# Kernel tuning notes

Measured on AMD Instinct MI355X. Metric: run time of the kernel, lower is better.

The kernel has to match this reference:

```python
import jax, jax.numpy as jnp
import numpy as np

B, S, E = 2, 2048, 2048
A, H = 2048, 16  # attention_dim, n_heads
HD = A // H      # head_dim = 128
ROPE_THETA = 10000.0


def setup_inputs() -> dict:
    key = jax.random.key(0)
    k1, k2, k3 = jax.random.split(key, 3)
    x = jax.random.normal(k1, (B, S, E), dtype=jnp.float32)
    W_qkv = jax.random.normal(k2, (E, 3 * A), dtype=jnp.float32) * 0.02
    W_out = jax.random.normal(k3, (A, E), dtype=jnp.float32) * 0.02
    return {"x": x, "W_qkv": W_qkv, "W_out": W_out}


def _apply_rope(x):
    # x: (B, H, S, D); interleaved rotary pairs (rotary-embedding-torch default)
    b, h, s, d = x.shape
    inv_freq = 1.0 / (ROPE_THETA ** (jnp.arange(0, d, 2, dtype=jnp.float32) / d))
    freqs = jnp.arange(s, dtype=jnp.float32)[:, None] * inv_freq[None, :]  # (S, D/2)
    cos, sin = jnp.cos(freqs), jnp.sin(freqs)
    xr = x.reshape(b, h, s, d // 2, 2)
    x1, x2 = xr[..., 0], xr[..., 1]
    o1 = x1 * cos - x2 * sin
    o2 = x1 * sin + x2 * cos
    return jnp.stack([o1, o2], axis=-1).reshape(b, h, s, d)


def reference(x, W_qkv, W_out):
    b, s, _ = x.shape
    qkv = (x @ W_qkv).reshape(b, s, 3, H, HD)          # (B,S,3,H,hd)
    qkv = jnp.moveaxis(qkv, 3, 1)                      # movedim(-2,1) -> (B,H,S,3,hd)
    q, k, v = qkv[..., 0, :], qkv[..., 1, :], qkv[..., 2, :]
    q = _apply_rope(q)
    k = _apply_rope(k)
    scale = 1.0 / jnp.sqrt(jnp.asarray(HD, dtype=x.dtype))
    scores = jnp.einsum("bhqd,bhkd->bhqk", q, k) * scale
    attn = jax.nn.softmax(scores, axis=-1)
    out = jnp.einsum("bhqk,bhkd->bhqd", attn, v)       # (B,H,S,hd)
    out = out.transpose(0, 2, 1, 3).reshape(b, s, A)   # (B,S,A)
    return out @ W_out
```

## Files before the change

### kernel.cpp

```cpp
#include <hip/hip_runtime.h>
#include <math.h>

typedef float  f32x4 __attribute__((ext_vector_type(4)));
typedef short  s16x8 __attribute__((ext_vector_type(8)));
typedef short  s16x4 __attribute__((ext_vector_type(4)));
typedef unsigned short u16;
typedef unsigned int u32;

static __device__ __forceinline__ u16 f32_to_bf16_rne(float f) {
    u32 u = __builtin_bit_cast(u32, f);
    u32 r = u + 0x7fffu + ((u >> 16) & 1u);
    return (u16)(r >> 16);
}
static __device__ __forceinline__ u32 pack_bf16_rhu(float a, float b) {
    u32 ua = __builtin_bit_cast(u32, a);
    u32 ub = __builtin_bit_cast(u32, b);
    return ((ua + 0x8000u) >> 16) | ((ub + 0x8000u) & 0xffff0000u);
}
static __device__ __forceinline__ float bf16_to_f32(u16 h) {
    return __builtin_bit_cast(float, (u32)h << 16);
}

static __device__ __forceinline__ void gl2lds16(const void* g, void* l) {
    __builtin_amdgcn_global_load_lds(
        (const __attribute__((address_space(1))) u32*)g,
        (__attribute__((address_space(3))) u32*)l, 16, 0, 0);
}

__global__ __launch_bounds__(256) void k_cast(const float* __restrict__ in,
                                              u16* __restrict__ out) {
    int i = (blockIdx.x * 256 + threadIdx.x) * 8;
    float4 a = *reinterpret_cast<const float4*>(in + i);
    float4 b = *reinterpret_cast<const float4*>(in + i + 4);
    s16x8 o;
    o[0] = (short)f32_to_bf16_rne(a.x); o[1] = (short)f32_to_bf16_rne(a.y);
    o[2] = (short)f32_to_bf16_rne(a.z); o[3] = (short)f32_to_bf16_rne(a.w);
    o[4] = (short)f32_to_bf16_rne(b.x); o[5] = (short)f32_to_bf16_rne(b.y);
    o[6] = (short)f32_to_bf16_rne(b.z); o[7] = (short)f32_to_bf16_rne(b.w);
    *reinterpret_cast<s16x8*>(out + i) = o;
}

__global__ __launch_bounds__(256) void k_transpose_cast(const float* __restrict__ in,
                                                        u16* __restrict__ out,
                                                        int R, int C) {
    __shared__ float TT[64 * 130];
    const int t = threadIdx.x;
    const int ct = blockIdx.x, rt = blockIdx.y;
    const int tr = t >> 4;
    const int tc = t & 15;
    float4 v[8];
#pragma unroll
    for (int u = 0; u < 8; ++u) {
        int r = u * 16 + tr;
        v[u] = *reinterpret_cast<const float4*>(in + (size_t)(rt * 128 + r) * C + ct * 64 + tc * 4);
    }
#pragma unroll
    for (int u = 0; u < 8; ++u) {
        int r = u * 16 + tr;
        TT[(tc * 4 + 0) * 130 + r] = v[u].x;
        TT[(tc * 4 + 1) * 130 + r] = v[u].y;
        TT[(tc * 4 + 2) * 130 + r] = v[u].z;
        TT[(tc * 4 + 3) * 130 + r] = v[u].w;
    }
    __syncthreads();
#pragma unroll
    for (int u = 0; u < 4; ++u) {
        int oc = u * 16 + tr;
        int r0 = tc * 8;
        s16x8 o;
#pragma unroll
        for (int e = 0; e < 8; ++e)
            o[e] = (short)f32_to_bf16_rne(TT[oc * 130 + r0 + e]);
        *reinterpret_cast<s16x8*>(out + (size_t)(ct * 64 + oc) * R + rt * 128 + r0) = o;
    }
}

template<bool BF16OUT, bool ROPE>
__global__ __launch_bounds__(256) void k_gemm_bt(const u16* __restrict__ Amat,
                                                 const u16* __restrict__ Bt,
                                                 void* __restrict__ Cout,
                                                 int M, int N, int K) {
    __shared__ __align__(16) u16 As[128 * 64];
    __shared__ __align__(16) u16 Bs[128 * 64];
    const int t = threadIdx.x;
    const int lane = t & 63, wave = t >> 6;
    const int m16 = lane & 15, qd = lane >> 4;
    const int wm = (wave >> 1) * 64, wn = (wave & 1) * 64;
    const size_t m0 = (size_t)blockIdx.y * 128, n0 = (size_t)blockIdx.x * 128;
    const int srow = lane >> 3;
    const int schunk = (lane & 7) ^ srow;

    f32x4 acc[4][4] = {};

    for (int k0 = 0; k0 < K; k0 += 64) {
#pragma unroll
        for (int j = 0; j < 4; ++j) {
            int rbase = j * 32 + wave * 8;
            int r = rbase + srow;
            gl2lds16(Amat + (m0 + r) * (size_t)K + k0 + schunk * 8, &As[rbase * 64]);
            gl2lds16(Bt   + (n0 + r) * (size_t)K + k0 + schunk * 8, &Bs[rbase * 64]);
        }
        __syncthreads();
#pragma unroll
        for (int kh = 0; kh < 2; ++kh) {
            s16x8 af[4], bf[4];
#pragma unroll
            for (int i = 0; i < 4; ++i) {
                int ra = wm + i * 16 + m16;
                int pa = (kh * 4 + qd) ^ (ra & 7);
                af[i] = *reinterpret_cast<const s16x8*>(&As[ra * 64 + pa * 8]);
                int rb = wn + i * 16 + m16;
                int pb = (kh * 4 + qd) ^ (rb & 7);
                bf[i] = *reinterpret_cast<const s16x8*>(&Bs[rb * 64 + pb * 8]);
            }
#pragma unroll
            for (int i = 0; i < 4; ++i)
#pragma unroll
                for (int jj = 0; jj < 4; ++jj)
                    acc[i][jj] = __builtin_amdgcn_mfma_f32_16x16x32_bf16(af[i], bf[jj], acc[i][jj], 0, 0, 0);
        }
        __syncthreads();
    }
    if (ROPE && n0 < 4096) {
        float invf[4];
#pragma unroll
        for (int j = 0; j < 4; ++j) {
            int pi = ((int)(wn + j * 16 + m16) & 127) >> 1;
            invf[j] = __expf(-0.14391156831f * (float)pi);
        }
#pragma unroll
        for (int i = 0; i < 4; ++i)
#pragma unroll
            for (int j = 0; j < 4; ++j)
#pragma unroll
                for (int r = 0; r < 4; ++r) {
                    float v = acc[i][j][r];
                    float p = __shfl_xor(v, 1);
                    size_t row = m0 + wm + i * 16 + qd * 4 + r;
                    float f = (float)(int)(row & 2047) * invf[j];
                    float sn, cs;
                    __sincosf(f, &sn, &cs);
                    float res = (m16 & 1) ? fmaf(p, sn, v * cs) : fmaf(v, cs, -p * sn);
                    size_t col = n0 + wn + j * 16 + m16;
                    ((u16*)Cout)[row * N + col] = f32_to_bf16_rne(res);
                }
    } else {
#pragma unroll
        for (int i = 0; i < 4; ++i)
#pragma unroll
            for (int j = 0; j < 4; ++j)
#pragma unroll
                for (int r = 0; r < 4; ++r) {
                    size_t row = m0 + wm + i * 16 + qd * 4 + r;
                    size_t col = n0 + wn + j * 16 + m16;
                    if (BF16OUT)
                        ((u16*)Cout)[row * N + col] = f32_to_bf16_rne(acc[i][j][r]);
                    else
                        ((float*)Cout)[row * N + col] = acc[i][j][r];
                }
    }
}

__global__ __launch_bounds__(256) void k_transpose_v(const u16* __restrict__ qkv,
                                                     u16* __restrict__ vt) {
    __shared__ u16 TT[128 * 130];
    const int t = threadIdx.x;
    const int st = blockIdx.x;
    const int bh = blockIdx.y;
    const int b = bh >> 4, h = bh & 15;
    const u16* src = qkv + (size_t)b * 2048 * 6144 + 4096 + (size_t)h * 128;
    const int tr = t >> 4, tc = t & 15;
    s16x8 v[8];
#pragma unroll
    for (int u = 0; u < 8; ++u) {
        int s = u * 16 + tr;
        v[u] = *reinterpret_cast<const s16x8*>(src + (size_t)(st * 128 + s) * 6144 + tc * 8);
    }
#pragma unroll
    for (int u = 0; u < 8; ++u) {
        int s = u * 16 + tr;
#pragma unroll
        for (int e = 0; e < 8; ++e)
            TT[(tc * 8 + e) * 130 + s] = (u16)v[u][e];
    }
    __syncthreads();
    u16* dst = vt + (size_t)bh * 128 * 2048 + st * 128;
#pragma unroll
    for (int u = 0; u < 8; ++u) {
        int d = u * 16 + tr;
        int s0 = tc * 8;
        s16x8 o;
#pragma unroll
        for (int e = 0; e < 8; ++e) o[e] = (short)TT[d * 130 + s0 + e];
        *reinterpret_cast<s16x8*>(dst + (size_t)d * 2048 + s0) = o;
    }
}

__global__ __launch_bounds__(512, 4) void k_flash(const u16* __restrict__ qkv,
                                                  const u16* __restrict__ vt,
                                                  u16* __restrict__ out) {
    __shared__ __align__(16) u16 KS[128 * 136];
    __shared__ __align__(16) u16 VS[128 * 136];
    const int t = threadIdx.x, lane = t & 63, wave = t >> 6;
    const int m16 = lane & 15, qd = lane >> 4;
    const int bh = blockIdx.y, b = bh >> 4, h = bh & 15;
    const int q0 = blockIdx.x * 128;
    const u16* Qg = qkv + (size_t)b * 2048 * 6144 + (size_t)h * 128;
    const u16* Kg = Qg + 2048;
    const u16* Vtg = vt + (size_t)bh * 128 * 2048;
    const float C2 = 0.12751743f;

    int srow[4], scol[4], pi0[4];
#pragma unroll
    for (int ci = 0; ci < 4; ++ci) {
        int idx = ci * 512 + t;
        int row = idx >> 4, c = idx & 15;
        srow[ci] = row;
        scol[ci] = c * 8;
        pi0[ci] = 32 * (c >> 2) + 16 * (c & 1) + 4 * ((c >> 1) & 1);
    }

    s16x8 qf[4];
#pragma unroll
    for (int kc = 0; kc < 4; ++kc)
        qf[kc] = *reinterpret_cast<const s16x8*>(
            Qg + (size_t)(q0 + wave * 16 + m16) * 6144 + kc * 32 + qd * 8);

    f32x4 accO[8] = {};
    float mrow = -1e30f, lrow = 0.f;

    for (int kt = 0; kt < 16; ++kt) {
        const int s0 = kt * 128;
        s16x8 kreg[4], vreg[4];
#pragma unroll
        for (int ci = 0; ci < 4; ++ci) {
            kreg[ci] = *reinterpret_cast<const s16x8*>(
                Kg + (size_t)(s0 + srow[ci]) * 6144 + scol[ci]);
            vreg[ci] = *reinterpret_cast<const s16x8*>(
                Vtg + (size_t)srow[ci] * 2048 + s0 + scol[ci]);
        }
        __syncthreads();
#pragma unroll
        for (int ci = 0; ci < 4; ++ci) {
            *reinterpret_cast<s16x8*>(&KS[srow[ci] * 136 + scol[ci]]) = kreg[ci];
            s16x4 lo = __builtin_shufflevector(vreg[ci], vreg[ci], 0, 1, 2, 3);
            s16x4 hi = __builtin_shufflevector(vreg[ci], vreg[ci], 4, 5, 6, 7);
            *reinterpret_cast<s16x4*>(&VS[srow[ci] * 136 + pi0[ci]]) = lo;
            *reinterpret_cast<s16x4*>(&VS[srow[ci] * 136 + pi0[ci] + 8]) = hi;
        }
        __syncthreads();

        f32x4 accS[8] = {};
#pragma unroll
        for (int kc = 0; kc < 4; ++kc)
#pragma unroll
            for (int nj = 0; nj < 8; ++nj) {
                s16x8 kf = *reinterpret_cast<const s16x8*>(
                    &KS[(nj * 16 + m16) * 136 + (kc * 4 + qd) * 8]);
                accS[nj] = __builtin_amdgcn_mfma_f32_16x16x32_bf16(kf, qf[kc], accS[nj], 0, 0, 0);
            }

        float mx = accS[0][0];
#pragma unroll
        for (int nj = 0; nj < 8; ++nj)
#pragma unroll
            for (int r = 0; r < 4; ++r) mx = fmaxf(mx, accS[nj][r]);
        mx *= C2;
        mx = fmaxf(mx, __shfl_xor(mx, 16));
        mx = fmaxf(mx, __shfl_xor(mx, 32));
        float mn = fmaxf(mrow, mx);
        float alpha = __builtin_amdgcn_exp2f(mrow - mn);
        mrow = mn;
        float ls = 0.f;
        s16x4 pk[8];
#pragma unroll
        for (int nj = 0; nj < 8; ++nj) {
            float p0 = __builtin_amdgcn_exp2f(fmaf(accS[nj][0], C2, -mn));
            float p1 = __builtin_amdgcn_exp2f(fmaf(accS[nj][1], C2, -mn));
            float p2 = __builtin_amdgcn_exp2f(fmaf(accS[nj][2], C2, -mn));
            float p3 = __builtin_amdgcn_exp2f(fmaf(accS[nj][3], C2, -mn));
            ls += (p0 + p1) + (p2 + p3);
            u32 lo = pack_bf16_rhu(p0, p1);
            u32 hi = pack_bf16_rhu(p2, p3);
            uint2 pr = make_uint2(lo, hi);
            pk[nj] = __builtin_bit_cast(s16x4, pr);
        }
        ls += __shfl_xor(ls, 16);
        ls += __shfl_xor(ls, 32);
        lrow = lrow * alpha + ls;
        float aO[4];
#pragma unroll
        for (int r = 0; r < 4; ++r) aO[r] = __shfl(alpha, qd * 4 + r);
#pragma unroll
        for (int dj = 0; dj < 8; ++dj)
#pragma unroll
            for (int r = 0; r < 4; ++r) accO[dj][r] *= aO[r];

#pragma unroll
        for (int kb = 0; kb < 4; ++kb) {
            s16x8 af = __builtin_shufflevector(pk[2 * kb], pk[2 * kb + 1],
                                               0, 1, 2, 3, 4, 5, 6, 7);
#pragma unroll
            for (int dj = 0; dj < 8; ++dj) {
                s16x8 vf = *reinterpret_cast<const s16x8*>(
                    &VS[(dj * 16 + m16) * 136 + kb * 32 + qd * 8]);
                accO[dj] = __builtin_amdgcn_mfma_f32_16x16x32_bf16(af, vf, accO[dj], 0, 0, 0);
            }
        }
    }
    float invl = 1.0f / lrow;
    float iv[4];
#pragma unroll
    for (int r = 0; r < 4; ++r) iv[r] = __shfl(invl, qd * 4 + r);
#pragma unroll
    for (int r = 0; r < 4; ++r) {
        size_t row = (size_t)b * 2048 + q0 + wave * 16 + qd * 4 + r;
#pragma unroll
        for (int dj = 0; dj < 8; ++dj)
            out[row * 2048 + h * 128 + dj * 16 + m16] =
                f32_to_bf16_rne(accO[dj][r] * iv[r]);
    }
}

extern "C" void kernel_launch(void* const* d_in, const int* in_sizes, int n_in,
                              void* d_out, int out_size, void* d_ws, size_t ws_size,
                              hipStream_t stream) {
    const float* x     = (const float*)d_in[0];
    const float* W_qkv = (const float*)d_in[1];
    const float* W_out = (const float*)d_in[2];
    float* out = (float*)d_out;

    char* ws = (char*)d_ws;
    u16* xb   = (u16*)(ws);
    u16* Wqt  = (u16*)(ws + (16u << 20));
    u16* Wot  = (u16*)(ws + (40u << 20));
    u16* qkvb = (u16*)(ws + (48u << 20));
    u16* attn = (u16*)(ws + (96u << 20));
    u16* vtg  = (u16*)(ws + (112u << 20));

    k_cast<<<4096, 256, 0, stream>>>(x, xb);
    k_transpose_cast<<<dim3(96, 16), 256, 0, stream>>>(W_qkv, Wqt, 2048, 6144);
    k_transpose_cast<<<dim3(32, 16), 256, 0, stream>>>(W_out, Wot, 2048, 2048);
    k_gemm_bt<true, true><<<dim3(48, 32), 256, 0, stream>>>(xb, Wqt, qkvb, 4096, 6144, 2048);
    k_transpose_v<<<dim3(16, 32), 256, 0, stream>>>(qkvb, vtg);
    k_flash<<<dim3(16, 32), 512, 0, stream>>>(qkvb, vtg, attn);
    k_gemm_bt<false, false><<<dim3(16, 32), 256, 0, stream>>>(attn, Wot, out, 4096, 2048, 2048);
}
```

Baseline: 409.3 us.

## Add 256x256-tile 8-wave GEMM with staged LDS pipeline for QKV projection

```diff
diff --git a/kernel.cpp b/kernel.cpp
--- a/kernel.cpp
+++ b/kernel.cpp
@@ -161,6 +161,187 @@
     }
 }
 
+template<bool BF16OUT, bool ROPE>
+__global__ __launch_bounds__(512) void k_gemm256(const u16* __restrict__ Amat,
+                                                 const u16* __restrict__ Bt,
+                                                 void* __restrict__ Cout,
+                                                 int M, int N, int K) {
+    __shared__ __align__(16) u16 As[2][256 * 64];
+    __shared__ __align__(16) u16 Bs[2][256 * 64];
+    const int t = threadIdx.x;
+    const int lane = t & 63, wave = t >> 6;
+    const int m16 = lane & 15, qd = lane >> 4;
+    const int wr = wave >> 2, wc = wave & 3;
+    const int srow = lane >> 3;
+    const int sch = (lane & 7) ^ srow;
+
+    const int nwg = gridDim.x * gridDim.y;
+    int orig = blockIdx.y * gridDim.x + blockIdx.x;
+    int qq = nwg >> 3, rr = nwg & 7;
+    int xcd = orig & 7, loc = orig >> 3;
+    int wg = (xcd < rr ? xcd * (qq + 1) : rr * (qq + 1) + (xcd - rr) * qq) + loc;
+    int bx = wg % gridDim.x, by = wg / gridDim.x;
+    const size_t m0 = (size_t)by * 256, n0 = (size_t)bx * 256;
+
+    const u16* Ab = Amat + m0 * (size_t)K;
+    const u16* Bb = Bt + n0 * (size_t)K;
+    const int NT = K >> 6;
+
+    auto stageA = [&](int p, int h, int k0) {
+        int rb0 = h * 128 + wave * 8;
+        gl2lds16(Ab + (size_t)(rb0 + srow) * K + k0 + sch * 8, &As[p][rb0 * 64]);
+        int rb1 = rb0 + 64;
+        gl2lds16(Ab + (size_t)(rb1 + srow) * K + k0 + sch * 8, &As[p][rb1 * 64]);
+    };
+    auto stageB = [&](int p, int h, int k0) {
+        int rb0 = h * 128 + wave * 8;
+        gl2lds16(Bb + (size_t)(rb0 + srow) * K + k0 + sch * 8, &Bs[p][rb0 * 64]);
+        int rb1 = rb0 + 64;
+        gl2lds16(Bb + (size_t)(rb1 + srow) * K + k0 + sch * 8, &Bs[p][rb1 * 64]);
+    };
+
+    f32x4 acc[8][4] = {};
+    s16x8 af[4][2], bq0[2][2], bq1[2][2];
+
+    stageA(0, 0, 0); stageA(0, 1, 0);
+    stageB(0, 0, 0); stageB(0, 1, 0);
+    if (NT > 1) {
+        stageB(1, 0, 64); stageB(1, 1, 64);
+        asm volatile("s_waitcnt vmcnt(4)" ::: "memory");
+    } else {
+        asm volatile("s_waitcnt vmcnt(0)" ::: "memory");
+    }
+    __builtin_amdgcn_s_barrier();
+
+    for (int kt = 0; kt < NT; ++kt) {
+        const int p = kt & 1;
+        const int rowA = wr * 128;
+
+#pragma unroll
+        for (int i = 0; i < 4; ++i) {
+            int ra = rowA + i * 16 + m16;
+            af[i][0] = *reinterpret_cast<const s16x8*>(&As[p][ra * 64 + ((qd)     ^ (ra & 7)) * 8]);
+            af[i][1] = *reinterpret_cast<const s16x8*>(&As[p][ra * 64 + ((4 + qd) ^ (ra & 7)) * 8]);
+        }
+#pragma unroll
+        for (int j = 0; j < 2; ++j) {
+            int rb = wc * 64 + j * 16 + m16;
+            bq0[j][0] = *reinterpret_cast<const s16x8*>(&Bs[p][rb * 64 + ((qd)     ^ (rb & 7)) * 8]);
+            bq0[j][1] = *reinterpret_cast<const s16x8*>(&Bs[p][rb * 64 + ((4 + qd) ^ (rb & 7)) * 8]);
+        }
+        if (kt + 1 < NT) stageA(p ^ 1, 0, (kt + 1) << 6);
+        __builtin_amdgcn_s_barrier();
+        asm volatile("s_waitcnt lgkmcnt(0)" ::: "memory");
+        __builtin_amdgcn_s_setprio(1);
+#pragma unroll
+        for (int i = 0; i < 4; ++i)
+#pragma unroll
+            for (int j = 0; j < 2; ++j) {
+                acc[i][j] = __builtin_amdgcn_mfma_f32_16x16x32_bf16(af[i][0], bq0[j][0], acc[i][j], 0, 0, 0);
+                acc[i][j] = __builtin_amdgcn_mfma_f32_16x16x32_bf16(af[i][1], bq0[j][1], acc[i][j], 0, 0, 0);
+            }
+        __builtin_amdgcn_s_setprio(0);
+        __builtin_amdgcn_s_barrier();
+
+#pragma unroll
+        for (int j = 0; j < 2; ++j) {
+            int rb = wc * 64 + 32 + j * 16 + m16;
+            bq1[j][0] = *reinterpret_cast<const s16x8*>(&Bs[p][rb * 64 + ((qd)     ^ (rb & 7)) * 8]);
+            bq1[j][1] = *reinterpret_cast<const s16x8*>(&Bs[p][rb * 64 + ((4 + qd) ^ (rb & 7)) * 8]);
+        }
+        if (kt + 1 < NT) stageA(p ^ 1, 1, (kt + 1) << 6);
+        __builtin_amdgcn_s_barrier();
+        asm volatile("s_waitcnt lgkmcnt(0)" ::: "memory");
+        __builtin_amdgcn_s_setprio(1);
+#pragma unroll
+        for (int i = 0; i < 4; ++i)
+#pragma unroll
+            for (int j = 0; j < 2; ++j) {
+                acc[i][2 + j] = __builtin_amdgcn_mfma_f32_16x16x32_bf16(af[i][0], bq1[j][0], acc[i][2 + j], 0, 0, 0);
+                acc[i][2 + j] = __builtin_amdgcn_mfma_f32_16x16x32_bf16(af[i][1], bq1[j][1], acc[i][2 + j], 0, 0, 0);
+            }
+        __builtin_amdgcn_s_setprio(0);
+        __builtin_amdgcn_s_barrier();
+
+#pragma unroll
+        for (int i = 0; i < 4; ++i) {
+            int ra = rowA + 64 + i * 16 + m16;
+            af[i][0] = *reinterpret_cast<const s16x8*>(&As[p][ra * 64 + ((qd)     ^ (ra & 7)) * 8]);
+            af[i][1] = *reinterpret_cast<const s16x8*>(&As[p][ra * 64 + ((4 + qd) ^ (ra & 7)) * 8]);
+        }
+        if (kt + 2 < NT) stageB(p, 0, (kt + 2) << 6);
+        __builtin_amdgcn_s_barrier();
+        asm volatile("s_waitcnt lgkmcnt(0)" ::: "memory");
+        __builtin_amdgcn_s_setprio(1);
+#pragma unroll
+        for (int i = 0; i < 4; ++i)
+#pragma unroll
+            for (int j = 0; j < 2; ++j) {
+                acc[4 + i][2 + j] = __builtin_amdgcn_mfma_f32_16x16x32_bf16(af[i][0], bq1[j][0], acc[4 + i][2 + j], 0, 0, 0);
+                acc[4 + i][2 + j] = __builtin_amdgcn_mfma_f32_16x16x32_bf16(af[i][1], bq1[j][1], acc[4 + i][2 + j], 0, 0, 0);
+            }
+        __builtin_amdgcn_s_setprio(0);
+        __builtin_amdgcn_s_barrier();
+
+        if (kt + 2 < NT) {
+            stageB(p, 1, (kt + 2) << 6);
+            asm volatile("s_waitcnt vmcnt(4)" ::: "memory");
+        } else {
+            asm volatile("s_waitcnt vmcnt(0)" ::: "memory");
+        }
+        __builtin_amdgcn_s_barrier();
+        __builtin_amdgcn_s_setprio(1);
+#pragma unroll
+        for (int i = 0; i < 4; ++i)
+#pragma unroll
+            for (int j = 0; j < 2; ++j) {
+                acc[4 + i][j] = __builtin_amdgcn_mfma_f32_16x16x32_bf16(af[i][0], bq0[j][0], acc[4 + i][j], 0, 0, 0);
+                acc[4 + i][j] = __builtin_amdgcn_mfma_f32_16x16x32_bf16(af[i][1], bq0[j][1], acc[4 + i][j], 0, 0, 0);
+            }
+        __builtin_amdgcn_s_setprio(0);
+        __builtin_amdgcn_s_barrier();
+    }
+
+    if (ROPE && n0 < 4096) {
+        float invf[4];
+#pragma unroll
+        for (int j = 0; j < 4; ++j) {
+            int pi = ((int)(wc * 64 + j * 16 + m16) & 127) >> 1;
+            invf[j] = __expf(-0.14391156831f * (float)pi);
+        }
+#pragma unroll
+        for (int i = 0; i < 8; ++i)
+#pragma unroll
+            for (int j = 0; j < 4; ++j)
+#pragma unroll
+                for (int r = 0; r < 4; ++r) {
+                    float v = acc[i][j][r];
+                    float pv = __shfl_xor(v, 1);
+                    size_t row = m0 + wr * 128 + i * 16 + qd * 4 + r;
+                    float f = (float)(int)(row & 2047) * invf[j];
+                    float sn, cs;
+                    __sincosf(f, &sn, &cs);
+                    float res = (m16 & 1) ? fmaf(pv, sn, v * cs) : fmaf(v, cs, -pv * sn);
+                    size_t col = n0 + wc * 64 + j * 16 + m16;
+                    ((u16*)Cout)[row * N + col] = f32_to_bf16_rne(res);
+                }
+    } else {
+#pragma unroll
+        for (int i = 0; i < 8; ++i)
+#pragma unroll
+            for (int j = 0; j < 4; ++j)
+#pragma unroll
+                for (int r = 0; r < 4; ++r) {
+                    size_t row = m0 + wr * 128 + i * 16 + qd * 4 + r;
+                    size_t col = n0 + wc * 64 + j * 16 + m16;
+                    if (BF16OUT)
+                        ((u16*)Cout)[row * N + col] = f32_to_bf16_rne(acc[i][j][r]);
+                    else
+                        ((float*)Cout)[row * N + col] = acc[i][j][r];
+                }
+    }
+}
+
 __global__ __launch_bounds__(256) void k_transpose_v(const u16* __restrict__ qkv,
                                                      u16* __restrict__ vt) {
     __shared__ u16 TT[128 * 130];
@@ -341,7 +522,7 @@
     k_cast<<<4096, 256, 0, stream>>>(x, xb);
     k_transpose_cast<<<dim3(96, 16), 256, 0, stream>>>(W_qkv, Wqt, 2048, 6144);
     k_transpose_cast<<<dim3(32, 16), 256, 0, stream>>>(W_out, Wot, 2048, 2048);
-    k_gemm_bt<true, true><<<dim3(48, 32), 256, 0, stream>>>(xb, Wqt, qkvb, 4096, 6144, 2048);
+    k_gemm256<true, true><<<dim3(24, 16), 512, 0, stream>>>(xb, Wqt, qkvb, 4096, 6144, 2048);
     k_transpose_v<<<dim3(16, 32), 256, 0, stream>>>(qkvb, vtg);
     k_flash<<<dim3(16, 32), 512, 0, stream>>>(qkvb, vtg, attn);
     k_gemm_bt<false, false><<<dim3(16, 32), 256, 0, stream>>>(attn, Wot, out, 4096, 2048, 2048);
```

Measured after the change: 411.3 us. Within noise of the previous version (+0.5%).
